# Kernel tuning notes

Measured on AMD Instinct MI355X. Metric: run time of the kernel, lower is better.

Reference implementation:

```python
import jax, jax.numpy as jnp
import numpy as np

B, S, H, E, K = 8, 4096, 1024, 256, 64
NEG = -1e30  # finite stand-in for -inf to keep grads NaN-free


def setup_inputs() -> dict:
    key = jax.random.key(0)
    ks = jax.random.split(key, 8)
    Hq = H // 4
    sc = 0.02
    return {
        "hidden_states": jax.random.normal(ks[0], (B, S, H), dtype=jnp.float32),
        "attention_mask": jnp.ones((B, S), dtype=jnp.int32),
        "block_boundaries": jnp.sort(jax.random.randint(ks[1], (B, K), 0, S), axis=-1),
        "tok_w1": jax.random.normal(ks[2], (H, Hq), dtype=jnp.float32) * sc,
        "tok_b1": jnp.zeros((Hq,), dtype=jnp.float32),
        "tok_w2": jax.random.normal(ks[3], (Hq, 1), dtype=jnp.float32) * sc,
        "tok_b2": jnp.zeros((1,), dtype=jnp.float32),
        "blk_w1": jax.random.normal(ks[4], (H, Hq), dtype=jnp.float32) * sc,
        "blk_b1": jnp.zeros((Hq,), dtype=jnp.float32),
        "blk_w2": jax.random.normal(ks[5], (Hq, 1), dtype=jnp.float32) * sc,
        "blk_b2": jnp.zeros((1,), dtype=jnp.float32),
        "out_w": jax.random.normal(ks[6], (H, E), dtype=jnp.float32) * sc,
        "out_b": jnp.zeros((E,), dtype=jnp.float32),
    }


def _attn_scores(x, w1, b1, w2, b2):
    # Linear -> Tanh -> Linear(.,1), squeeze last dim
    return (jnp.tanh(x @ w1 + b1) @ w2 + b2)[..., 0]


def reference(hidden_states, attention_mask, block_boundaries,
              tok_w1, tok_b1, tok_w2, tok_b2,
              blk_w1, blk_b1, blk_w2, blk_b2,
              out_w, out_b):
    Bz, Sz, Hz = hidden_states.shape
    Kz = block_boundaries.shape[1]
    pos = jnp.arange(Sz)
    # token -> block id: last boundary <= pos (tokens before first boundary get -1)
    block_id = jax.vmap(lambda bnd: jnp.searchsorted(bnd, pos, side='right') - 1)(block_boundaries)  # [B,S]
    member = block_id[:, :, None] == jnp.arange(Kz)[None, None, :]      # [B,S,K]
    valid = (attention_mask == 1) & (block_id >= 0)                     # [B,S]
    m_full = member & valid[:, :, None]                                 # [B,S,K]

    # stage 1: per-block masked softmax over tokens
    tok_scores = _attn_scores(hidden_states, tok_w1, tok_b1, tok_w2, tok_b2)  # [B,S]
    s = jnp.where(m_full, tok_scores[:, :, None], NEG)
    mx = jnp.max(s, axis=1, keepdims=True)                              # [B,1,K]
    e = jnp.where(m_full, jnp.exp(tok_scores[:, :, None] - mx), 0.0)
    denom = jnp.sum(e, axis=1, keepdims=True)                           # [B,1,K]
    w = jnp.where(denom > 0, e / jnp.maximum(denom, 1e-30), 0.0)
    block_embed = jnp.einsum('bsk,bsd->bkd', w, hidden_states)          # [B,K,H]
    block_valid = denom[:, 0, :] > 0                                    # [B,K] (empty blocks dropped)

    # stage 2: softmax over (non-empty) blocks
    blk_scores = _attn_scores(block_embed, blk_w1, blk_b1, blk_w2, blk_b2)    # [B,K]
    blk_scores = jnp.where(block_valid, blk_scores, NEG)
    bw = jax.nn.softmax(blk_scores, axis=-1)
    func = jnp.einsum('bk,bkd->bd', bw, block_embed)                    # [B,H]

    out = func @ out_w + out_b                                          # [B,E]
    return out / jnp.maximum(jnp.linalg.norm(out, axis=-1, keepdims=True), 1e-12)
```

## Files before the change

kernel.cpp:

```cpp
#include <hip/hip_runtime.h>
#include <math.h>

#define BB 8
#define SS 4096
#define HH 1024
#define EE 256
#define KK 64
#define HQ 256
#define NEGF -1e30f

typedef short bf16x8 __attribute__((ext_vector_type(8)));
typedef float f32x4  __attribute__((ext_vector_type(4)));

__device__ inline short f2bf(float x) {
    unsigned u = __float_as_uint(x);
    unsigned r = (u + 0x7fffu + ((u >> 16) & 1u)) >> 16;
    return (short)r;
}

__global__ __launch_bounds__(256) void convert_w1_kernel(
    const float* __restrict__ w1, short* __restrict__ w1s)
{
    const int kb = blockIdx.x, n = threadIdx.x;
    for (int kk = 0; kk < 32; kk++)
        w1s[kb * 8192 + n * 32 + kk] = f2bf(w1[(kb * 32 + kk) * HQ + n]);
}

__global__ __launch_bounds__(256) void mfma_score_kernel(
    const float* __restrict__ X, const short* __restrict__ w1s,
    const float* __restrict__ b1, const float* __restrict__ w2,
    const float* __restrict__ b2, float* __restrict__ out)
{
    __shared__ __attribute__((aligned(16))) short xs[64 * 40];
    __shared__ __attribute__((aligned(16))) short wsx[256 * 40];
    __shared__ float part[4][64];

    const int t = threadIdx.x;
    const int wv = t >> 6, lane = t & 63, lo = lane & 15, q = lane >> 4;
    const long row0 = (long)blockIdx.x * 64;

    const int srow = t >> 2, skg = (t & 3) * 8;
    const float* xrow = X + (row0 + srow) * HH;

    f32x4 acc[4][4];
#pragma unroll
    for (int i = 0; i < 4; i++)
#pragma unroll
        for (int j = 0; j < 4; j++) acc[i][j] = (f32x4){0.f, 0.f, 0.f, 0.f};

    for (int kb = 0; kb < 32; kb++) {
        __syncthreads();
        {
            const float4* p = (const float4*)(xrow + kb * 32 + skg);
            float4 v0 = p[0], v1 = p[1];
            bf16x8 pk;
            pk[0] = f2bf(v0.x); pk[1] = f2bf(v0.y); pk[2] = f2bf(v0.z); pk[3] = f2bf(v0.w);
            pk[4] = f2bf(v1.x); pk[5] = f2bf(v1.y); pk[6] = f2bf(v1.z); pk[7] = f2bf(v1.w);
            *(bf16x8*)(xs + srow * 40 + skg) = pk;
            const uint4* src = (const uint4*)(w1s + kb * 8192 + t * 32);
            uint4 a0 = src[0], a1 = src[1], a2 = src[2], a3 = src[3];
            uint4* dst = (uint4*)(wsx + t * 40);
            dst[0] = a0; dst[1] = a1; dst[2] = a2; dst[3] = a3;
        }
        __syncthreads();

        bf16x8 af[4], bfr[4];
#pragma unroll
        for (int rt = 0; rt < 4; rt++)
            af[rt] = *(bf16x8*)(xs + (rt * 16 + lo) * 40 + q * 8);
#pragma unroll
        for (int ct = 0; ct < 4; ct++)
            bfr[ct] = *(bf16x8*)(wsx + (wv * 64 + ct * 16 + lo) * 40 + q * 8);
#pragma unroll
        for (int rt = 0; rt < 4; rt++)
#pragma unroll
            for (int ct = 0; ct < 4; ct++)
                acc[rt][ct] = __builtin_amdgcn_mfma_f32_16x16x32_bf16(
                    af[rt], bfr[ct], acc[rt][ct], 0, 0, 0);
    }

    float rowpart[4][4];
#pragma unroll
    for (int rt = 0; rt < 4; rt++)
#pragma unroll
        for (int r = 0; r < 4; r++) rowpart[rt][r] = 0.f;
#pragma unroll
    for (int ct = 0; ct < 4; ct++) {
        const int c = wv * 64 + ct * 16 + lo;
        const float b1c = b1[c], w2c = w2[c];
#pragma unroll
        for (int rt = 0; rt < 4; rt++)
#pragma unroll
            for (int r = 0; r < 4; r++)
                rowpart[rt][r] += tanhf(acc[rt][ct][r] + b1c) * w2c;
    }
#pragma unroll
    for (int rt = 0; rt < 4; rt++)
#pragma unroll
        for (int r = 0; r < 4; r++) {
            float v = rowpart[rt][r];
            v += __shfl_down(v, 8, 64);
            v += __shfl_down(v, 4, 64);
            v += __shfl_down(v, 2, 64);
            v += __shfl_down(v, 1, 64);
            rowpart[rt][r] = v;
        }
    if (lo == 0)
#pragma unroll
        for (int rt = 0; rt < 4; rt++)
#pragma unroll
            for (int r = 0; r < 4; r++)
                part[wv][rt * 16 + q * 4 + r] = rowpart[rt][r];
    __syncthreads();
    if (t < 64)
        out[row0 + t] = part[0][t] + part[1][t] + part[2][t] + part[3][t] + b2[0];
}

__global__ __launch_bounds__(256) void block_stats_kernel(
    const float* __restrict__ scores, const int* __restrict__ mask,
    const int* __restrict__ bnd, float* __restrict__ bmax, float* __restrict__ bden,
    float* __restrict__ wtok)
{
    const int b = blockIdx.x >> 6, k = blockIdx.x & 63;
    const int start = bnd[b * KK + k];
    const int end = (k == KK - 1) ? SS : bnd[b * KK + k + 1];
    const int tid = threadIdx.x;
    __shared__ float r[4];
    __shared__ float mshared, dshared;

    float m = NEGF;
    for (int s = start + tid; s < end; s += 256)
        if (mask[b * SS + s] == 1) m = fmaxf(m, scores[b * SS + s]);
    for (int off = 32; off > 0; off >>= 1) m = fmaxf(m, __shfl_down(m, off, 64));
    if ((tid & 63) == 0) r[tid >> 6] = m;
    __syncthreads();
    if (tid == 0) mshared = fmaxf(fmaxf(r[0], r[1]), fmaxf(r[2], r[3]));
    __syncthreads();
    m = mshared;

    float d = 0.f;
    for (int s = start + tid; s < end; s += 256)
        if (mask[b * SS + s] == 1) d += expf(scores[b * SS + s] - m);
    for (int off = 32; off > 0; off >>= 1) d += __shfl_down(d, off, 64);
    __syncthreads();
    if ((tid & 63) == 0) r[tid >> 6] = d;
    __syncthreads();
    if (tid == 0) {
        float den = r[0] + r[1] + r[2] + r[3];
        bmax[blockIdx.x] = m; bden[blockIdx.x] = den;
        dshared = (den > 0.f) ? 1.f / fmaxf(den, 1e-30f) : 0.f;
    }
    __syncthreads();
    const float inv = dshared;
    for (int s = start + tid; s < end; s += 256)
        wtok[b * SS + s] = (mask[b * SS + s] == 1) ? expf(scores[b * SS + s] - m) * inv : 0.f;
}

#define TCH 32
__global__ __launch_bounds__(256) void block_embed2_kernel(
    const float* __restrict__ hidden, const float* __restrict__ wtok,
    const int* __restrict__ bnd, float* __restrict__ embed)
{
    const int b = blockIdx.x >> 7;
    const int ch = blockIdx.x & 127;
    const int t = threadIdx.x;
    __shared__ int bsh[KK];
    if (t < KK) bsh[t] = bnd[b * KK + t];
    __syncthreads();

    const int s0 = ch * TCH, s1 = s0 + TCH;
    int cur = -1;
    for (int i = 0; i < KK; i++) if (bsh[i] <= s0) cur = i;

    float a0 = 0.f, a1 = 0.f, a2 = 0.f, a3 = 0.f;
    bool any = false;
    for (int s = s0; s < s1; s++) {
        while (cur + 1 < KK && bsh[cur + 1] <= s) {
            if (any) {
                float* e = embed + ((long)b * KK + cur) * HH;
                atomicAdd(e + t, a0); atomicAdd(e + t + 256, a1);
                atomicAdd(e + t + 512, a2); atomicAdd(e + t + 768, a3);
                a0 = a1 = a2 = a3 = 0.f; any = false;
            }
            cur++;
        }
        if (cur < 0) continue;
        const float w = wtok[b * SS + s];
        if (w != 0.f) {
            const float* hr = hidden + ((long)b * SS + s) * HH;
            a0 = fmaf(w, hr[t], a0);
            a1 = fmaf(w, hr[t + 256], a1);
            a2 = fmaf(w, hr[t + 512], a2);
            a3 = fmaf(w, hr[t + 768], a3);
            any = true;
        }
    }
    if (any) {
        float* e = embed + ((long)b * KK + cur) * HH;
        atomicAdd(e + t, a0); atomicAdd(e + t + 256, a1);
        atomicAdd(e + t + 512, a2); atomicAdd(e + t + 768, a3);
    }
}

__global__ __launch_bounds__(1024) void finalize_kernel(
    const float* __restrict__ embed, const float* __restrict__ bscores,
    const float* __restrict__ bden, const float* __restrict__ out_w,
    const float* __restrict__ out_b, float* __restrict__ outp)
{
    const int b = blockIdx.x, tid = threadIdx.x;
    __shared__ float bw[KK];
    __shared__ float func[HH];
    __shared__ float red[4][EE];
    __shared__ float osh[EE];
    __shared__ float r4[4];

    if (tid < KK) {
        float s = (bden[b * KK + tid] > 0.f) ? bscores[b * KK + tid] : NEGF;
        float m = s;
        for (int off = 32; off > 0; off >>= 1) m = fmaxf(m, __shfl_xor(m, off, 64));
        float e = expf(s - m);
        float d = e;
        for (int off = 32; off > 0; off >>= 1) d += __shfl_xor(d, off, 64);
        bw[tid] = e / d;
    }
    __syncthreads();

    {
        float f = 0.f;
        const float* ep = embed + (long)b * KK * HH + tid;
#pragma unroll
        for (int k = 0; k < KK; k++)
            f = fmaf(bw[k], ep[(long)k * HH], f);
        func[tid] = f;
    }
    __syncthreads();

    {
        const int e = tid & 255, hc = tid >> 8;
        float o = 0.f;
        const float* wp = out_w + (long)hc * 256 * EE + e;
#pragma unroll 8
        for (int h = 0; h < 256; h++)
            o = fmaf(func[hc * 256 + h], wp[(long)h * EE], o);
        red[hc][e] = o;
    }
    __syncthreads();

    if (tid < 256) {
        float oo = red[0][tid] + red[1][tid] + red[2][tid] + red[3][tid] + out_b[tid];
        osh[tid] = oo;
        float sq = oo * oo;
        for (int off = 32; off > 0; off >>= 1) sq += __shfl_down(sq, off, 64);
        if ((tid & 63) == 0) r4[tid >> 6] = sq;
    }
    __syncthreads();
    if (tid < 256) {
        const float nrm = sqrtf(r4[0] + r4[1] + r4[2] + r4[3]);
        outp[b * EE + tid] = osh[tid] / fmaxf(nrm, 1e-12f);
    }
}

extern "C" void kernel_launch(void* const* d_in, const int* in_sizes, int n_in,
                              void* d_out, int out_size, void* d_ws, size_t ws_size,
                              hipStream_t stream) {
    const float* hidden  = (const float*)d_in[0];
    const int*   mask    = (const int*)  d_in[1];
    const int*   bnd     = (const int*)  d_in[2];
    const float* tok_w1  = (const float*)d_in[3];
    const float* tok_b1  = (const float*)d_in[4];
    const float* tok_w2  = (const float*)d_in[5];
    const float* tok_b2  = (const float*)d_in[6];
    const float* blk_w1  = (const float*)d_in[7];
    const float* blk_b1  = (const float*)d_in[8];
    const float* blk_w2  = (const float*)d_in[9];
    const float* blk_b2  = (const float*)d_in[10];
    const float* out_w   = (const float*)d_in[11];
    const float* out_b   = (const float*)d_in[12];

    float* ws      = (float*)d_ws;
    float* wtok    = ws;
    float* embed   = ws + 32768;
    float* scores  = ws + 557056;
    float* bmax    = ws + 589824;
    float* bden    = ws + 590336;
    float* bscores = ws + 590848;
    short* w1s     = (short*)(ws + 591360);

    hipMemsetAsync(d_ws, 0, (size_t)557056 * 4, stream);

    convert_w1_kernel<<<32, 256, 0, stream>>>(tok_w1, w1s);
    mfma_score_kernel<<<BB * SS / 64, 256, 0, stream>>>(
        hidden, w1s, tok_b1, tok_w2, tok_b2, scores);
    block_stats_kernel<<<BB * KK, 256, 0, stream>>>(scores, mask, bnd, bmax, bden, wtok);
    block_embed2_kernel<<<BB * SS / TCH, 256, 0, stream>>>(hidden, wtok, bnd, embed);
    convert_w1_kernel<<<32, 256, 0, stream>>>(blk_w1, w1s);
    mfma_score_kernel<<<BB * KK / 64, 256, 0, stream>>>(
        embed, w1s, blk_b1, blk_w2, blk_b2, bscores);
    finalize_kernel<<<BB, 1024, 0, stream>>>(
        embed, bscores, bden, out_w, out_b, (float*)d_out);
}
```

Before: 328.3 us.

## Load MFMA operands directly from global, vectorize block embed, split finalize

The score GEMM kernel now reads X and the pre-converted weights straight from global memory into MFMA fragment registers. This drops the LDS staging and both barriers per K step, and it converts to bf16 with a cheaper round-half-up packing. The block-embed kernel uses float4 loads, smaller token chunks for more blocks, and unconditional FMAs instead of skipping zero weights. The single-block-per-batch finalize is split into three kernels, with the output projection spread over more blocks via atomics. The risks are uncoalesced global loads in the GEMM, more launches, and slightly different bf16 rounding.

```diff
diff --git a/kernel.cpp b/kernel.cpp
--- a/kernel.cpp
+++ b/kernel.cpp
@@ -18,6 +18,12 @@
     return (short)r;
 }
 
+__device__ inline unsigned pk2bf(float lo, float hi) {
+    unsigned a = __float_as_uint(lo) + 0x8000u;
+    unsigned b = __float_as_uint(hi) + 0x8000u;
+    return (a >> 16) | (b & 0xffff0000u);
+}
+
 __global__ __launch_bounds__(256) void convert_w1_kernel(
     const float* __restrict__ w1, short* __restrict__ w1s)
 {
@@ -26,51 +32,42 @@
         w1s[kb * 8192 + n * 32 + kk] = f2bf(w1[(kb * 32 + kk) * HQ + n]);
 }
 
-__global__ __launch_bounds__(256) void mfma_score_kernel(
+__global__ __launch_bounds__(256) void mfma_score2_kernel(
     const float* __restrict__ X, const short* __restrict__ w1s,
     const float* __restrict__ b1, const float* __restrict__ w2,
     const float* __restrict__ b2, float* __restrict__ out)
 {
-    __shared__ __attribute__((aligned(16))) short xs[64 * 40];
-    __shared__ __attribute__((aligned(16))) short wsx[256 * 40];
     __shared__ float part[4][64];
-
     const int t = threadIdx.x;
     const int wv = t >> 6, lane = t & 63, lo = lane & 15, q = lane >> 4;
     const long row0 = (long)blockIdx.x * 64;
 
-    const int srow = t >> 2, skg = (t & 3) * 8;
-    const float* xrow = X + (row0 + srow) * HH;
-
     f32x4 acc[4][4];
 #pragma unroll
     for (int i = 0; i < 4; i++)
 #pragma unroll
         for (int j = 0; j < 4; j++) acc[i][j] = (f32x4){0.f, 0.f, 0.f, 0.f};
 
+    const float* xp = X + (row0 + lo) * HH + q * 8;
+    const short* wp = w1s + (wv * 64 + lo) * 32 + q * 8;
+
     for (int kb = 0; kb < 32; kb++) {
-        __syncthreads();
-        {
-            const float4* p = (const float4*)(xrow + kb * 32 + skg);
+        bf16x8 bfr[4];
+#pragma unroll
+        for (int ct = 0; ct < 4; ct++)
+            bfr[ct] = *(const bf16x8*)(wp + kb * 8192 + ct * 512);
+        bf16x8 af[4];
+#pragma unroll
+        for (int rt = 0; rt < 4; rt++) {
+            const float4* p = (const float4*)(xp + (long)rt * 16 * HH + kb * 32);
             float4 v0 = p[0], v1 = p[1];
-            bf16x8 pk;
-            pk[0] = f2bf(v0.x); pk[1] = f2bf(v0.y); pk[2] = f2bf(v0.z); pk[3] = f2bf(v0.w);
-            pk[4] = f2bf(v1.x); pk[5] = f2bf(v1.y); pk[6] = f2bf(v1.z); pk[7] = f2bf(v1.w);
-            *(bf16x8*)(xs + srow * 40 + skg) = pk;
-            const uint4* src = (const uint4*)(w1s + kb * 8192 + t * 32);
-            uint4 a0 = src[0], a1 = src[1], a2 = src[2], a3 = src[3];
-            uint4* dst = (uint4*)(wsx + t * 40);
-            dst[0] = a0; dst[1] = a1; dst[2] = a2; dst[3] = a3;
+            union { unsigned u[4]; bf16x8 h; } c;
+            c.u[0] = pk2bf(v0.x, v0.y);
+            c.u[1] = pk2bf(v0.z, v0.w);
+            c.u[2] = pk2bf(v1.x, v1.y);
+            c.u[3] = pk2bf(v1.z, v1.w);
+            af[rt] = c.h;
         }
-        __syncthreads();
-
-        bf16x8 af[4], bfr[4];
-#pragma unroll
-        for (int rt = 0; rt < 4; rt++)
-            af[rt] = *(bf16x8*)(xs + (rt * 16 + lo) * 40 + q * 8);
-#pragma unroll
-        for (int ct = 0; ct < 4; ct++)
-            bfr[ct] = *(bf16x8*)(wsx + (wv * 64 + ct * 16 + lo) * 40 + q * 8);
 #pragma unroll
         for (int rt = 0; rt < 4; rt++)
 #pragma unroll
@@ -156,108 +153,110 @@
         wtok[b * SS + s] = (mask[b * SS + s] == 1) ? expf(scores[b * SS + s] - m) * inv : 0.f;
 }
 
-#define TCH 32
-__global__ __launch_bounds__(256) void block_embed2_kernel(
+#define TCH 16
+__global__ __launch_bounds__(256) void block_embed3_kernel(
     const float* __restrict__ hidden, const float* __restrict__ wtok,
     const int* __restrict__ bnd, float* __restrict__ embed)
 {
-    const int b = blockIdx.x >> 7;
-    const int ch = blockIdx.x & 127;
+    const int b = blockIdx.x >> 8;
+    const int ch = blockIdx.x & 255;
     const int t = threadIdx.x;
     __shared__ int bsh[KK];
     if (t < KK) bsh[t] = bnd[b * KK + t];
     __syncthreads();
 
-    const int s0 = ch * TCH, s1 = s0 + TCH;
+    const int s0 = ch * TCH;
     int cur = -1;
-    for (int i = 0; i < KK; i++) if (bsh[i] <= s0) cur = i;
-
-    float a0 = 0.f, a1 = 0.f, a2 = 0.f, a3 = 0.f;
+#pragma unroll
+    for (int i = 0; i < KK; i++) cur = (bsh[i] <= s0) ? i : cur;
+
+    float4 a = {0.f, 0.f, 0.f, 0.f};
     bool any = false;
-    for (int s = s0; s < s1; s++) {
+    const float4* hp = (const float4*)(hidden + ((long)b * SS + s0) * HH) + t;
+    const float* wt = wtok + b * SS + s0;
+
+    for (int i = 0; i < TCH; i++) {
+        const int s = s0 + i;
         while (cur + 1 < KK && bsh[cur + 1] <= s) {
             if (any) {
-                float* e = embed + ((long)b * KK + cur) * HH;
-                atomicAdd(e + t, a0); atomicAdd(e + t + 256, a1);
-                atomicAdd(e + t + 512, a2); atomicAdd(e + t + 768, a3);
-                a0 = a1 = a2 = a3 = 0.f; any = false;
+                float* e = embed + ((long)b * KK + cur) * HH + t * 4;
+                atomicAdd(e, a.x); atomicAdd(e + 1, a.y);
+                atomicAdd(e + 2, a.z); atomicAdd(e + 3, a.w);
+                a = (float4){0.f, 0.f, 0.f, 0.f}; any = false;
             }
             cur++;
         }
-        if (cur < 0) continue;
-        const float w = wtok[b * SS + s];
-        if (w != 0.f) {
-            const float* hr = hidden + ((long)b * SS + s) * HH;
-            a0 = fmaf(w, hr[t], a0);
-            a1 = fmaf(w, hr[t + 256], a1);
-            a2 = fmaf(w, hr[t + 512], a2);
-            a3 = fmaf(w, hr[t + 768], a3);
-            any = true;
-        }
+        const float w = wt[i];
+        const float4 h = hp[i * (HH / 4)];
+        a.x = fmaf(w, h.x, a.x); a.y = fmaf(w, h.y, a.y);
+        a.z = fmaf(w, h.z, a.z); a.w = fmaf(w, h.w, a.w);
+        any = any | (w != 0.f);
     }
     if (any) {
-        float* e = embed + ((long)b * KK + cur) * HH;
-        atomicAdd(e + t, a0); atomicAdd(e + t + 256, a1);
-        atomicAdd(e + t + 512, a2); atomicAdd(e + t + 768, a3);
-    }
-}
-
-__global__ __launch_bounds__(1024) void finalize_kernel(
+        float* e = embed + ((long)b * KK + cur) * HH + t * 4;
+        atomicAdd(e, a.x); atomicAdd(e + 1, a.y);
+        atomicAdd(e + 2, a.z); atomicAdd(e + 3, a.w);
+    }
+}
+
+__global__ __launch_bounds__(256) void finalize_a_kernel(
     const float* __restrict__ embed, const float* __restrict__ bscores,
-    const float* __restrict__ bden, const float* __restrict__ out_w,
-    const float* __restrict__ out_b, float* __restrict__ outp)
-{
-    const int b = blockIdx.x, tid = threadIdx.x;
+    const float* __restrict__ bden, float* __restrict__ func)
+{
+    const int b = blockIdx.x, t = threadIdx.x;
     __shared__ float bw[KK];
-    __shared__ float func[HH];
-    __shared__ float red[4][EE];
-    __shared__ float osh[EE];
-    __shared__ float r4[4];
-
-    if (tid < KK) {
-        float s = (bden[b * KK + tid] > 0.f) ? bscores[b * KK + tid] : NEGF;
+    if (t < KK) {
+        float s = (bden[b * KK + t] > 0.f) ? bscores[b * KK + t] : NEGF;
         float m = s;
         for (int off = 32; off > 0; off >>= 1) m = fmaxf(m, __shfl_xor(m, off, 64));
         float e = expf(s - m);
         float d = e;
         for (int off = 32; off > 0; off >>= 1) d += __shfl_xor(d, off, 64);
-        bw[tid] = e / d;
-    }
-    __syncthreads();
-
-    {
-        float f = 0.f;
-        const float* ep = embed + (long)b * KK * HH + tid;
-#pragma unroll
-        for (int k = 0; k < KK; k++)
-            f = fmaf(bw[k], ep[(long)k * HH], f);
-        func[tid] = f;
-    }
-    __syncthreads();
-
-    {
-        const int e = tid & 255, hc = tid >> 8;
-        float o = 0.f;
-        const float* wp = out_w + (long)hc * 256 * EE + e;
+        bw[t] = e / d;
+    }
+    __syncthreads();
+    float4 f = {0.f, 0.f, 0.f, 0.f};
+    const float4* ep = (const float4*)(embed + (long)b * KK * HH) + t;
 #pragma unroll 8
-        for (int h = 0; h < 256; h++)
-            o = fmaf(func[hc * 256 + h], wp[(long)h * EE], o);
-        red[hc][e] = o;
-    }
-    __syncthreads();
-
-    if (tid < 256) {
-        float oo = red[0][tid] + red[1][tid] + red[2][tid] + red[3][tid] + out_b[tid];
-        osh[tid] = oo;
-        float sq = oo * oo;
-        for (int off = 32; off > 0; off >>= 1) sq += __shfl_down(sq, off, 64);
-        if ((tid & 63) == 0) r4[tid >> 6] = sq;
-    }
-    __syncthreads();
-    if (tid < 256) {
-        const float nrm = sqrtf(r4[0] + r4[1] + r4[2] + r4[3]);
-        outp[b * EE + tid] = osh[tid] / fmaxf(nrm, 1e-12f);
-    }
+    for (int k = 0; k < KK; k++) {
+        const float w = bw[k];
+        const float4 h = ep[k * (HH / 4)];
+        f.x = fmaf(w, h.x, f.x); f.y = fmaf(w, h.y, f.y);
+        f.z = fmaf(w, h.z, f.z); f.w = fmaf(w, h.w, f.w);
+    }
+    *((float4*)(func + b * HH) + t) = f;
+}
+
+__global__ __launch_bounds__(256) void finalize_b_kernel(
+    const float* __restrict__ func, const float* __restrict__ out_w,
+    float* __restrict__ osum)
+{
+    const int b = blockIdx.x >> 3, hc = blockIdx.x & 7;
+    const int t = threadIdx.x;
+    __shared__ float fsh[128];
+    if (t < 128) fsh[t] = func[b * HH + hc * 128 + t];
+    __syncthreads();
+    float acc = 0.f;
+    const float* wp = out_w + (long)(hc * 128) * EE + t;
+#pragma unroll 8
+    for (int h = 0; h < 128; h++)
+        acc = fmaf(fsh[h], wp[(long)h * EE], acc);
+    atomicAdd(&osum[b * EE + t], acc);
+}
+
+__global__ __launch_bounds__(256) void finalize_c_kernel(
+    const float* __restrict__ osum, const float* __restrict__ out_b,
+    float* __restrict__ outp)
+{
+    const int b = blockIdx.x, t = threadIdx.x;
+    __shared__ float r4[4];
+    float o = osum[b * EE + t] + out_b[t];
+    float sq = o * o;
+    for (int off = 32; off > 0; off >>= 1) sq += __shfl_down(sq, off, 64);
+    if ((t & 63) == 0) r4[t >> 6] = sq;
+    __syncthreads();
+    const float nrm = sqrtf(r4[0] + r4[1] + r4[2] + r4[3]);
+    outp[b * EE + t] = o / fmaxf(nrm, 1e-12f);
 }
 
 extern "C" void kernel_launch(void* const* d_in, const int* in_sizes, int n_in,
@@ -280,22 +279,25 @@
     float* ws      = (float*)d_ws;
     float* wtok    = ws;
     float* embed   = ws + 32768;
-    float* scores  = ws + 557056;
-    float* bmax    = ws + 589824;
-    float* bden    = ws + 590336;
-    float* bscores = ws + 590848;
-    short* w1s     = (short*)(ws + 591360);
-
-    hipMemsetAsync(d_ws, 0, (size_t)557056 * 4, stream);
+    float* osum    = ws + 557056;
+    float* scores  = ws + 559104;
+    float* bmax    = ws + 591872;
+    float* bden    = ws + 592384;
+    float* bscores = ws + 592896;
+    float* func    = ws + 593408;
+    short* w1s     = (short*)(ws + 601600);
+
+    hipMemsetAsync(d_ws, 0, (size_t)559104 * 4, stream);
 
     convert_w1_kernel<<<32, 256, 0, stream>>>(tok_w1, w1s);
-    mfma_score_kernel<<<BB * SS / 64, 256, 0, stream>>>(
+    mfma_score2_kernel<<<BB * SS / 64, 256, 0, stream>>>(
         hidden, w1s, tok_b1, tok_w2, tok_b2, scores);
     block_stats_kernel<<<BB * KK, 256, 0, stream>>>(scores, mask, bnd, bmax, bden, wtok);
-    block_embed2_kernel<<<BB * SS / TCH, 256, 0, stream>>>(hidden, wtok, bnd, embed);
+    block_embed3_kernel<<<BB * SS / TCH, 256, 0, stream>>>(hidden, wtok, bnd, embed);
     convert_w1_kernel<<<32, 256, 0, stream>>>(blk_w1, w1s);
-    mfma_score_kernel<<<BB * KK / 64, 256, 0, stream>>>(
+    mfma_score2_kernel<<<BB * KK / 64, 256, 0, stream>>>(
         embed, w1s, blk_b1, blk_w2, blk_b2, bscores);
-    finalize_kernel<<<BB, 1024, 0, stream>>>(
-        embed, bscores, bden, out_w, out_b, (float*)d_out);
-}
+    finalize_a_kernel<<<BB, 256, 0, stream>>>(embed, bscores, bden, func);
+    finalize_b_kernel<<<BB * 8, 256, 0, stream>>>(func, out_w, osum);
+    finalize_c_kernel<<<BB, 256, 0, stream>>>(osum, out_b, (float*)d_out);
+}
```

Result: slower. 370.2 us (+12.8%).
